# Optimization experiments

Measured on AMD Instinct MI355X. Metric: run time of the kernel, lower is better.

## Reference

```python
import jax, jax.numpy as jnp
import numpy as np

SQRT2 = np.float32(np.sqrt(2.0))


def _depthwise(x, h, axis):
    """Symmetric-pad depthwise 1D conv along `axis` (2=col/height, 3=row/width).
    Emulates dtcwt_slim ColFilter/RowFilter: prep_filt flips the taps, then
    F.conv2d cross-correlates with groups=C (same taps for every channel).
    x: (B,C,H,W), h: (L,) with L odd -> same-size output."""
    C = x.shape[1]
    L = h.shape[0]
    m = L // 2
    hf = jnp.flip(h)  # prep_filt stores h[::-1]
    if axis == 2:
        xp = jnp.pad(x, ((0, 0), (0, 0), (m, m), (0, 0)), mode='symmetric')
        ker = jnp.tile(hf[None, None, :, None], (C, 1, 1, 1))  # (C,1,L,1)
    else:
        xp = jnp.pad(x, ((0, 0), (0, 0), (0, 0), (m, m)), mode='symmetric')
        ker = jnp.tile(hf[None, None, None, :], (C, 1, 1, 1))  # (C,1,1,L)
    return jax.lax.conv_general_dilated(
        xp, ker, window_strides=(1, 1), padding='VALID',
        dimension_numbers=('NCHW', 'OIHW', 'NCHW'), feature_group_count=C)


def colfilter(x, h):
    return _depthwise(x, h, axis=2)


def rowfilter(x, h):
    return _depthwise(x, h, axis=3)


def c2q(w_r, w_i):
    """Complex pair of subbands -> real quad-interleaved image.
    w_r, w_i: (B,C,2,H,W) -> (B,C,2H,2W)."""
    w1r, w1i = w_r[:, :, 0], w_i[:, :, 0]
    w2r, w2i = w_r[:, :, 1], w_i[:, :, 1]
    x1 = w1r + w2r          # y[::2,  ::2]
    x2 = w1i + w2i          # y[::2, 1::2]
    x3 = w1i - w2i          # y[1::2, ::2]
    x4 = w2r - w1r          # y[1::2,1::2]
    B, C, H, W = x1.shape
    top = jnp.stack([x1, x2], axis=-1).reshape(B, C, H, 2 * W)
    bot = jnp.stack([x3, x4], axis=-1).reshape(B, C, H, 2 * W)
    y = jnp.stack([top, bot], axis=-2).reshape(B, C, 2 * H, 2 * W)
    return y / SQRT2


def setup_inputs() -> dict:
    key = jax.random.key(0)
    k1, k2, k3, k4, k5, k6 = jax.random.split(key, 6)
    B, C, H, W = 8, 64, 256, 256
    Yl = jax.random.normal(k1, (B, C, H, W), dtype=jnp.float32)
    Yhr = jax.random.normal(k2, (B, C, 6, H // 2, W // 2), dtype=jnp.float32)
    Yhi = jax.random.normal(k3, (B, C, 6, H // 2, W // 2), dtype=jnp.float32)
    # near_sym_b_bp synthesis filters (fixed, non-trainable buffers): 13/19/13 taps
    g0o = jax.random.normal(k4, (13,), dtype=jnp.float32) * 0.3
    g1o = jax.random.normal(k5, (19,), dtype=jnp.float32) * 0.3
    g2o = jax.random.normal(k6, (13,), dtype=jnp.float32) * 0.3
    return {"Yl": Yl, "Yhr": Yhr, "Yhi": Yhi, "g0o": g0o, "g1o": g1o, "g2o": g2o}


def reference(Yl, Yhr, Yhi, g0o, g1o, g2o):
    # orientation pairs: (15,165)->lh uses bands 0,5; (75,105)->hl bands 2,3;
    # (45,135 bandpass)->hh bands 1,4
    lh = c2q(Yhr[:, :, 0:6:5], Yhi[:, :, 0:6:5])
    hl = c2q(Yhr[:, :, 2:4:1], Yhi[:, :, 2:4:1])
    hh = c2q(Yhr[:, :, 1:5:3], Yhi[:, :, 1:5:3])
    y1 = colfilter(Yl, g0o) + colfilter(lh, g1o)
    y2 = colfilter(hl, g0o)
    y2bp = colfilter(hh, g2o)
    y = rowfilter(y1, g0o) + rowfilter(y2, g1o) + rowfilter(y2bp, g2o)
    return y
```

## Files before the change

### kernel.cpp

```cpp
#include <hip/hip_runtime.h>

#define TH 32
#define TW 64
#define PW 88

__device__ __forceinline__ int symidx(int t, int n) {
    t = (t < 0) ? (-1 - t) : t;
    return (t >= n) ? (2 * n - 1 - t) : t;
}

__device__ __forceinline__ void col13_yl(
    float (&acc)[TH], const float* __restrict__ ylp,
    const float (&taps)[13], int r0, int cc)
{
    #pragma unroll
    for (int pi = 0; pi < TH + 12; ++pi) {
        int rr = symidx(r0 - 6 + pi, 256);
        float v = ylp[rr * 256 + cc];
        #pragma unroll
        for (int j = 0; j < 13; ++j) {
            int ro = pi + j - 12;
            if (ro >= 0 && ro < TH) acc[ro] = fmaf(taps[j], v, acc[ro]);
        }
    }
}

__device__ __forceinline__ void col13_c2q(
    float (&acc)[TH], const float* __restrict__ yhr, const float* __restrict__ yhi,
    int bA, int bB, const float (&taps)[13], int r0, int cc)
{
    const int cp = cc & 1;
    const int j2 = cc >> 1;
    const float IS2 = 0.70710678118654752f;
    #pragma unroll
    for (int pi = 0; pi < TH + 12; ++pi) {
        int rr = symidx(r0 - 6 + pi, 256);
        int rp = rr & 1;
        int i2 = rr >> 1;
        const float* base = (((rp ^ cp) != 0) ? yhi : yhr) + (i2 * 128 + j2);
        float A  = base[bA * 16384];
        float Bv = base[bB * 16384];
        float vA = (rp & cp)       ? -A  : A;
        float vB = (rp & (cp ^ 1)) ? -Bv : Bv;
        float v = (vA + vB) * IS2;
        #pragma unroll
        for (int j = 0; j < 13; ++j) {
            int ro = pi + j - 12;
            if (ro >= 0 && ro < TH) acc[ro] = fmaf(taps[j], v, acc[ro]);
        }
    }
}

__device__ __forceinline__ void col19_c2q(
    float (&acc)[TH], const float* __restrict__ yhr, const float* __restrict__ yhi,
    const float (&taps)[19], int r0, int cc)
{
    const int bA = 0, bB = 5;
    const int cp = cc & 1;
    const int j2 = cc >> 1;
    const float IS2 = 0.70710678118654752f;
    #pragma unroll
    for (int pi = 0; pi < TH + 18; ++pi) {
        int rr = symidx(r0 - 9 + pi, 256);
        int rp = rr & 1;
        int i2 = rr >> 1;
        const float* base = (((rp ^ cp) != 0) ? yhi : yhr) + (i2 * 128 + j2);
        float A  = base[bA * 16384];
        float Bv = base[bB * 16384];
        float vA = (rp & cp)       ? -A  : A;
        float vB = (rp & (cp ^ 1)) ? -Bv : Bv;
        float v = (vA + vB) * IS2;
        #pragma unroll
        for (int j = 0; j < 19; ++j) {
            int ro = pi + j - 18;
            if (ro >= 0 && ro < TH) acc[ro] = fmaf(taps[j], v, acc[ro]);
        }
    }
}

extern "C" __global__ __launch_bounds__(512) void dtcwt_inv(
    const float* __restrict__ Yl, const float* __restrict__ Yhr,
    const float* __restrict__ Yhi,
    const float* __restrict__ g0, const float* __restrict__ g1,
    const float* __restrict__ g2, float* __restrict__ out)
{
    __shared__ __align__(16) float sT[4][TH][PW];

    const int tid = threadIdx.x;
    const int plane = blockIdx.z;
    const int r0 = blockIdx.y * TH;
    const int c0 = blockIdx.x * TW;

    const float* ylp = Yl  + (size_t)plane * 65536;
    const float* yhr = Yhr + (size_t)plane * 6 * 16384;
    const float* yhi = Yhi + (size_t)plane * 6 * 16384;

    float G0[13], G1[19], G2[13];
    #pragma unroll
    for (int j = 0; j < 13; ++j) G0[j] = g0[j];
    #pragma unroll
    for (int j = 0; j < 19; ++j) G1[j] = g1[j];
    #pragma unroll
    for (int j = 0; j < 13; ++j) G2[j] = g2[j];

    const int role = tid >> 7;
    const int lr   = tid & 127;

    float acc[TH];
    #pragma unroll
    for (int i = 0; i < TH; ++i) acc[i] = 0.0f;

    int ti = -1;
    if (role == 0) {
        if (lr < 76) {
            ti = lr + 6;
            int cc = symidx(c0 + ti - 12, 256);
            col13_yl(acc, ylp, G0, r0, cc);
        }
    } else if (role == 1) {
        if (lr < 76) {
            ti = lr + 6;
            int cc = symidx(c0 + ti - 12, 256);
            col19_c2q(acc, yhr, yhi, G1, r0, cc);
        }
    } else if (role == 2) {
        if (lr < 82) {
            ti = lr + 3;
            int cc = symidx(c0 + ti - 12, 256);
            col13_c2q(acc, yhr, yhi, 2, 3, G0, r0, cc);
        }
    } else {
        if (lr < 76) {
            ti = lr + 6;
            int cc = symidx(c0 + ti - 12, 256);
            col13_c2q(acc, yhr, yhi, 1, 4, G2, r0, cc);
        }
    }
    if (ti >= 0) {
        #pragma unroll
        for (int ro = 0; ro < TH; ++ro) sT[role][ro][ti] = acc[ro];
    }
    __syncthreads();

    const int cg = tid & 15;
    const int r  = tid >> 4;
    const int cb = 4 * cg;

    float w1[20];
    #pragma unroll
    for (int k = 0; k < 5; ++k) {
        float4 a = *(const float4*)&sT[0][r][cb + 4 + 4 * k];
        float4 b = *(const float4*)&sT[1][r][cb + 4 + 4 * k];
        w1[4*k+0] = a.x + b.x; w1[4*k+1] = a.y + b.y;
        w1[4*k+2] = a.z + b.z; w1[4*k+3] = a.w + b.w;
    }
    float w2[28];
    #pragma unroll
    for (int k = 0; k < 7; ++k) {
        float4 a = *(const float4*)&sT[2][r][cb + 4 * k];
        w2[4*k+0] = a.x; w2[4*k+1] = a.y; w2[4*k+2] = a.z; w2[4*k+3] = a.w;
    }
    float w3[20];
    #pragma unroll
    for (int k = 0; k < 5; ++k) {
        float4 a = *(const float4*)&sT[3][r][cb + 4 + 4 * k];
        w3[4*k+0] = a.x; w3[4*k+1] = a.y; w3[4*k+2] = a.z; w3[4*k+3] = a.w;
    }

    float4 res;
    float* rp = (float*)&res;
    #pragma unroll
    for (int q = 0; q < 4; ++q) {
        float s = 0.0f;
        #pragma unroll
        for (int j = 0; j < 13; ++j) s = fmaf(G0[j], w1[q + 14 - j], s);
        #pragma unroll
        for (int j = 0; j < 19; ++j) s = fmaf(G1[j], w2[q + 21 - j], s);
        #pragma unroll
        for (int j = 0; j < 13; ++j) s = fmaf(G2[j], w3[q + 14 - j], s);
        rp[q] = s;
    }
    *(float4*)&out[(size_t)plane * 65536 + (size_t)(r0 + r) * 256 + (c0 + cb)] = res;
}

extern "C" void kernel_launch(void* const* d_in, const int* in_sizes, int n_in,
                              void* d_out, int out_size, void* d_ws, size_t ws_size,
                              hipStream_t stream) {
    const float* Yl  = (const float*)d_in[0];
    const float* Yhr = (const float*)d_in[1];
    const float* Yhi = (const float*)d_in[2];
    const float* g0  = (const float*)d_in[3];
    const float* g1  = (const float*)d_in[4];
    const float* g2  = (const float*)d_in[5];
    float* out = (float*)d_out;

    dim3 grid(256 / TW, 256 / TH, 8 * 64);
    dim3 block(512, 1, 1);
    dtcwt_inv<<<grid, block, 0, stream>>>(Yl, Yhr, Yhi, g0, g1, g2, out);
}
```

Baseline: 351.2 us.

## Add interior-row fast path computing column pairs per thread with shared c2q loads

For row tiles away from the image border, each thread now computes two adjacent columns. For Yl it loads float2 pairs. For the c2q subbands it loads each of the four complex values once and reuses them for both row parities and both column parities, which removes the per-row symmetric indexing and repeated gathers. Filter taps are read directly from global memory instead of being copied into register arrays, which lowers register pressure but may add scalar loads. Border tiles keep the original path. Each active thread now holds two 32-element accumulator arrays, which raises register use, and only about 38 to 42 of the 64 threads in each of four waves do work.

```diff
diff --git a/kernel.cpp b/kernel.cpp
--- a/kernel.cpp
+++ b/kernel.cpp
@@ -3,6 +3,7 @@
 #define TH 32
 #define TW 64
 #define PW 88
+#define IS2 0.70710678118654752f
 
 __device__ __forceinline__ int symidx(int t, int n) {
     t = (t < 0) ? (-1 - t) : t;
@@ -11,7 +12,7 @@
 
 __device__ __forceinline__ void col13_yl(
     float (&acc)[TH], const float* __restrict__ ylp,
-    const float (&taps)[13], int r0, int cc)
+    const float* __restrict__ taps, int r0, int cc)
 {
     #pragma unroll
     for (int pi = 0; pi < TH + 12; ++pi) {
@@ -27,11 +28,10 @@
 
 __device__ __forceinline__ void col13_c2q(
     float (&acc)[TH], const float* __restrict__ yhr, const float* __restrict__ yhi,
-    int bA, int bB, const float (&taps)[13], int r0, int cc)
+    int bA, int bB, const float* __restrict__ taps, int r0, int cc)
 {
     const int cp = cc & 1;
     const int j2 = cc >> 1;
-    const float IS2 = 0.70710678118654752f;
     #pragma unroll
     for (int pi = 0; pi < TH + 12; ++pi) {
         int rr = symidx(r0 - 6 + pi, 256);
@@ -53,12 +53,11 @@
 
 __device__ __forceinline__ void col19_c2q(
     float (&acc)[TH], const float* __restrict__ yhr, const float* __restrict__ yhi,
-    const float (&taps)[19], int r0, int cc)
+    const float* __restrict__ taps, int r0, int cc)
 {
     const int bA = 0, bB = 5;
     const int cp = cc & 1;
     const int j2 = cc >> 1;
-    const float IS2 = 0.70710678118654752f;
     #pragma unroll
     for (int pi = 0; pi < TH + 18; ++pi) {
         int rr = symidx(r0 - 9 + pi, 256);
@@ -78,6 +77,62 @@
     }
 }
 
+template<int L, int NP, int EPI0>
+__device__ __forceinline__ void c2q_col_fast(
+    float (&accE)[TH], float (&accO)[TH],
+    const float* __restrict__ pRA, const float* __restrict__ pRB,
+    const float* __restrict__ pIA, const float* __restrict__ pIB,
+    int vof, const float* __restrict__ taps)
+{
+    #pragma unroll
+    for (int u = 0; u < NP; ++u) {
+        float Ar = pRA[vof + u * 128];
+        float Br = pRB[vof + u * 128];
+        float Ai = pIA[vof + u * 128];
+        float Bi = pIB[vof + u * 128];
+        float cee = (Ar + Br) * IS2;
+        float coe = (Ai + Bi) * IS2;
+        float ceo = (Ai - Bi) * IS2;
+        float coo = (Br - Ar) * IS2;
+        const int piE = EPI0 + 2 * u;
+        #pragma unroll
+        for (int j = 0; j < L; ++j) {
+            int ro = piE + j - (L - 1);
+            if (ro >= 0 && ro < TH) {
+                accE[ro] = fmaf(taps[j], cee, accE[ro]);
+                accO[ro] = fmaf(taps[j], coe, accO[ro]);
+            }
+        }
+        #pragma unroll
+        for (int j = 0; j < L; ++j) {
+            int ro = piE + 1 + j - (L - 1);
+            if (ro >= 0 && ro < TH) {
+                accE[ro] = fmaf(taps[j], ceo, accE[ro]);
+                accO[ro] = fmaf(taps[j], coo, accO[ro]);
+            }
+        }
+    }
+}
+
+__device__ __forceinline__ void yl_col_fast(
+    float (&accX)[TH], float (&accY)[TH],
+    const float* __restrict__ ylp, int rbase, int lo,
+    const float* __restrict__ taps)
+{
+    #pragma unroll
+    for (int pi = 0; pi < TH + 12; ++pi) {
+        float2 v = *(const float2*)&ylp[(rbase + pi) * 256 + lo];
+        #pragma unroll
+        for (int j = 0; j < 13; ++j) {
+            int ro = pi + j - 12;
+            if (ro >= 0 && ro < TH) {
+                accX[ro] = fmaf(taps[j], v.x, accX[ro]);
+                accY[ro] = fmaf(taps[j], v.y, accY[ro]);
+            }
+        }
+    }
+}
+
 extern "C" __global__ __launch_bounds__(512) void dtcwt_inv(
     const float* __restrict__ Yl, const float* __restrict__ Yhr,
     const float* __restrict__ Yhi,
@@ -95,50 +150,126 @@
     const float* yhr = Yhr + (size_t)plane * 6 * 16384;
     const float* yhi = Yhi + (size_t)plane * 6 * 16384;
 
-    float G0[13], G1[19], G2[13];
-    #pragma unroll
-    for (int j = 0; j < 13; ++j) G0[j] = g0[j];
-    #pragma unroll
-    for (int j = 0; j < 19; ++j) G1[j] = g1[j];
-    #pragma unroll
-    for (int j = 0; j < 13; ++j) G2[j] = g2[j];
-
-    const int role = tid >> 7;
-    const int lr   = tid & 127;
-
-    float acc[TH];
-    #pragma unroll
-    for (int i = 0; i < TH; ++i) acc[i] = 0.0f;
-
-    int ti = -1;
-    if (role == 0) {
-        if (lr < 76) {
-            ti = lr + 6;
-            int cc = symidx(c0 + ti - 12, 256);
-            col13_yl(acc, ylp, G0, r0, cc);
-        }
-    } else if (role == 1) {
-        if (lr < 76) {
-            ti = lr + 6;
-            int cc = symidx(c0 + ti - 12, 256);
-            col19_c2q(acc, yhr, yhi, G1, r0, cc);
-        }
-    } else if (role == 2) {
-        if (lr < 82) {
-            ti = lr + 3;
-            int cc = symidx(c0 + ti - 12, 256);
-            col13_c2q(acc, yhr, yhi, 2, 3, G0, r0, cc);
+    const bool rowInterior = (blockIdx.y >= 1) && (blockIdx.y <= 6);
+
+    if (rowInterior) {
+        const int w = tid >> 6;
+        const int p = tid & 63;
+        if (w == 0) {
+            if (p < 38) {
+                int e0 = c0 - 6 + 2 * p;
+                int s0 = symidx(e0, 256);
+                int s1 = symidx(e0 + 1, 256);
+                int lo = (s0 < s1) ? s0 : s1;
+                float accX[TH], accY[TH];
+                #pragma unroll
+                for (int i = 0; i < TH; ++i) { accX[i] = 0.f; accY[i] = 0.f; }
+                yl_col_fast(accX, accY, ylp, r0 - 6, lo, g0);
+                int ti0 = 6 + 2 * p;
+                int sw = (s0 == lo) ? 0 : 1;
+                #pragma unroll
+                for (int ro = 0; ro < TH; ++ro) {
+                    sT[0][ro][ti0 + sw]     = accX[ro];
+                    sT[0][ro][ti0 + 1 - sw] = accY[ro];
+                }
+            }
+        } else if (w == 1) {
+            if (p < 38) {
+                int e0 = c0 - 6 + 2 * p;
+                int s0 = symidx(e0, 256);
+                int j2 = s0 >> 1;
+                int q0 = s0 & 1;
+                float accE[TH], accO[TH];
+                #pragma unroll
+                for (int i = 0; i < TH; ++i) { accE[i] = 0.f; accO[i] = 0.f; }
+                int vof = ((r0 - 10) >> 1) * 128 + j2;
+                c2q_col_fast<19, 26, -1>(accE, accO,
+                    yhr + 0 * 16384, yhr + 5 * 16384,
+                    yhi + 0 * 16384, yhi + 5 * 16384, vof, g1);
+                int ti0 = 6 + 2 * p;
+                #pragma unroll
+                for (int ro = 0; ro < TH; ++ro) {
+                    sT[1][ro][ti0 + q0]     = accE[ro];
+                    sT[1][ro][ti0 + 1 - q0] = accO[ro];
+                }
+            }
+        } else if (w == 2) {
+            if (p < 42) {
+                int e0 = c0 - 10 + 2 * p;
+                int s0 = symidx(e0, 256);
+                int j2 = s0 >> 1;
+                int q0 = s0 & 1;
+                float accE[TH], accO[TH];
+                #pragma unroll
+                for (int i = 0; i < TH; ++i) { accE[i] = 0.f; accO[i] = 0.f; }
+                int vof = ((r0 - 6) >> 1) * 128 + j2;
+                c2q_col_fast<13, 22, 0>(accE, accO,
+                    yhr + 2 * 16384, yhr + 3 * 16384,
+                    yhi + 2 * 16384, yhi + 3 * 16384, vof, g0);
+                int ti0 = 2 + 2 * p;
+                #pragma unroll
+                for (int ro = 0; ro < TH; ++ro) {
+                    sT[2][ro][ti0 + q0]     = accE[ro];
+                    sT[2][ro][ti0 + 1 - q0] = accO[ro];
+                }
+            }
+        } else if (w == 3) {
+            if (p < 38) {
+                int e0 = c0 - 6 + 2 * p;
+                int s0 = symidx(e0, 256);
+                int j2 = s0 >> 1;
+                int q0 = s0 & 1;
+                float accE[TH], accO[TH];
+                #pragma unroll
+                for (int i = 0; i < TH; ++i) { accE[i] = 0.f; accO[i] = 0.f; }
+                int vof = ((r0 - 6) >> 1) * 128 + j2;
+                c2q_col_fast<13, 22, 0>(accE, accO,
+                    yhr + 1 * 16384, yhr + 4 * 16384,
+                    yhi + 1 * 16384, yhi + 4 * 16384, vof, g2);
+                int ti0 = 6 + 2 * p;
+                #pragma unroll
+                for (int ro = 0; ro < TH; ++ro) {
+                    sT[3][ro][ti0 + q0]     = accE[ro];
+                    sT[3][ro][ti0 + 1 - q0] = accO[ro];
+                }
+            }
         }
     } else {
-        if (lr < 76) {
-            ti = lr + 6;
-            int cc = symidx(c0 + ti - 12, 256);
-            col13_c2q(acc, yhr, yhi, 1, 4, G2, r0, cc);
-        }
-    }
-    if (ti >= 0) {
-        #pragma unroll
-        for (int ro = 0; ro < TH; ++ro) sT[role][ro][ti] = acc[ro];
+        const int role = tid >> 7;
+        const int lr   = tid & 127;
+        float acc[TH];
+        #pragma unroll
+        for (int i = 0; i < TH; ++i) acc[i] = 0.0f;
+        int ti = -1;
+        if (role == 0) {
+            if (lr < 76) {
+                ti = lr + 6;
+                int cc = symidx(c0 + ti - 12, 256);
+                col13_yl(acc, ylp, g0, r0, cc);
+            }
+        } else if (role == 1) {
+            if (lr < 76) {
+                ti = lr + 6;
+                int cc = symidx(c0 + ti - 12, 256);
+                col19_c2q(acc, yhr, yhi, g1, r0, cc);
+            }
+        } else if (role == 2) {
+            if (lr < 82) {
+                ti = lr + 3;
+                int cc = symidx(c0 + ti - 12, 256);
+                col13_c2q(acc, yhr, yhi, 2, 3, g0, r0, cc);
+            }
+        } else {
+            if (lr < 76) {
+                ti = lr + 6;
+                int cc = symidx(c0 + ti - 12, 256);
+                col13_c2q(acc, yhr, yhi, 1, 4, g2, r0, cc);
+            }
+        }
+        if (ti >= 0) {
+            #pragma unroll
+            for (int ro = 0; ro < TH; ++ro) sT[role][ro][ti] = acc[ro];
+        }
     }
     __syncthreads();
 
@@ -173,11 +304,11 @@
     for (int q = 0; q < 4; ++q) {
         float s = 0.0f;
         #pragma unroll
-        for (int j = 0; j < 13; ++j) s = fmaf(G0[j], w1[q + 14 - j], s);
-        #pragma unroll
-        for (int j = 0; j < 19; ++j) s = fmaf(G1[j], w2[q + 21 - j], s);
-        #pragma unroll
-        for (int j = 0; j < 13; ++j) s = fmaf(G2[j], w3[q + 14 - j], s);
+        for (int j = 0; j < 13; ++j) s = fmaf(g0[j], w1[q + 14 - j], s);
+        #pragma unroll
+        for (int j = 0; j < 19; ++j) s = fmaf(g1[j], w2[q + 21 - j], s);
+        #pragma unroll
+        for (int j = 0; j < 13; ++j) s = fmaf(g2[j], w3[q + 14 - j], s);
         rp[q] = s;
     }
     *(float4*)&out[(size_t)plane * 65536 + (size_t)(r0 + r) * 256 + (c0 + cb)] = res;
```

After: 440.4 us. 1.25x slower.

## Add interior-row fast path without symmetric index math for column filters

Applied to the files above, without the earlier changes.

Blocks whose row range is away from the image border (tile rows 1-6) now take a specialised column-filter path. It drops the per-row symmetric-index computation and the per-element yhr/yhi selects, and processes c2q rows in even/odd pairs with fixed pointers and a sign factor. Filter taps are read directly from global memory (uniform loads) instead of being cached in register arrays, which may lower register pressure. The cost is larger code and a second, divergent-by-block path that must stay consistent with the border path.

```diff
diff --git a/kernel.cpp b/kernel.cpp
--- a/kernel.cpp
+++ b/kernel.cpp
@@ -3,6 +3,7 @@
 #define TH 32
 #define TW 64
 #define PW 88
+#define IS2 0.70710678118654752f
 
 __device__ __forceinline__ int symidx(int t, int n) {
     t = (t < 0) ? (-1 - t) : t;
@@ -11,7 +12,7 @@
 
 __device__ __forceinline__ void col13_yl(
     float (&acc)[TH], const float* __restrict__ ylp,
-    const float (&taps)[13], int r0, int cc)
+    const float* __restrict__ taps, int r0, int cc)
 {
     #pragma unroll
     for (int pi = 0; pi < TH + 12; ++pi) {
@@ -27,11 +28,10 @@
 
 __device__ __forceinline__ void col13_c2q(
     float (&acc)[TH], const float* __restrict__ yhr, const float* __restrict__ yhi,
-    int bA, int bB, const float (&taps)[13], int r0, int cc)
+    int bA, int bB, const float* __restrict__ taps, int r0, int cc)
 {
     const int cp = cc & 1;
     const int j2 = cc >> 1;
-    const float IS2 = 0.70710678118654752f;
     #pragma unroll
     for (int pi = 0; pi < TH + 12; ++pi) {
         int rr = symidx(r0 - 6 + pi, 256);
@@ -53,12 +53,11 @@
 
 __device__ __forceinline__ void col19_c2q(
     float (&acc)[TH], const float* __restrict__ yhr, const float* __restrict__ yhi,
-    const float (&taps)[19], int r0, int cc)
+    const float* __restrict__ taps, int r0, int cc)
 {
     const int bA = 0, bB = 5;
     const int cp = cc & 1;
     const int j2 = cc >> 1;
-    const float IS2 = 0.70710678118654752f;
     #pragma unroll
     for (int pi = 0; pi < TH + 18; ++pi) {
         int rr = symidx(r0 - 9 + pi, 256);
@@ -78,6 +77,34 @@
     }
 }
 
+template<int L, int NP, int EPI0>
+__device__ __forceinline__ void c2q_col_fast1(
+    float (&acc)[TH],
+    const float* __restrict__ pEA, const float* __restrict__ pEB,
+    const float* __restrict__ pOA, const float* __restrict__ pOB,
+    int vof, float sgn, const float* __restrict__ taps)
+{
+    #pragma unroll
+    for (int u = 0; u < NP; ++u) {
+        float Ae = pEA[vof + u * 128];
+        float Be = pEB[vof + u * 128];
+        float Ao = pOA[vof + u * 128];
+        float Bo = pOB[vof + u * 128];
+        float ve = (Ae + Be) * IS2;
+        float vo = (Ao - Bo) * sgn;
+        #pragma unroll
+        for (int j = 0; j < L; ++j) {
+            int ro = EPI0 + 2 * u + j - (L - 1);
+            if (ro >= 0 && ro < TH) acc[ro] = fmaf(taps[j], ve, acc[ro]);
+        }
+        #pragma unroll
+        for (int j = 0; j < L; ++j) {
+            int ro = EPI0 + 2 * u + 1 + j - (L - 1);
+            if (ro >= 0 && ro < TH) acc[ro] = fmaf(taps[j], vo, acc[ro]);
+        }
+    }
+}
+
 extern "C" __global__ __launch_bounds__(512) void dtcwt_inv(
     const float* __restrict__ Yl, const float* __restrict__ Yhr,
     const float* __restrict__ Yhi,
@@ -95,13 +122,7 @@
     const float* yhr = Yhr + (size_t)plane * 6 * 16384;
     const float* yhi = Yhi + (size_t)plane * 6 * 16384;
 
-    float G0[13], G1[19], G2[13];
-    #pragma unroll
-    for (int j = 0; j < 13; ++j) G0[j] = g0[j];
-    #pragma unroll
-    for (int j = 0; j < 19; ++j) G1[j] = g1[j];
-    #pragma unroll
-    for (int j = 0; j < 13; ++j) G2[j] = g2[j];
+    const bool rowInterior = (blockIdx.y >= 1) && (blockIdx.y <= 6);
 
     const int role = tid >> 7;
     const int lr   = tid & 127;
@@ -109,31 +130,89 @@
     float acc[TH];
     #pragma unroll
     for (int i = 0; i < TH; ++i) acc[i] = 0.0f;
-
     int ti = -1;
-    if (role == 0) {
-        if (lr < 76) {
-            ti = lr + 6;
-            int cc = symidx(c0 + ti - 12, 256);
-            col13_yl(acc, ylp, G0, r0, cc);
-        }
-    } else if (role == 1) {
-        if (lr < 76) {
-            ti = lr + 6;
-            int cc = symidx(c0 + ti - 12, 256);
-            col19_c2q(acc, yhr, yhi, G1, r0, cc);
-        }
-    } else if (role == 2) {
-        if (lr < 82) {
-            ti = lr + 3;
-            int cc = symidx(c0 + ti - 12, 256);
-            col13_c2q(acc, yhr, yhi, 2, 3, G0, r0, cc);
+
+    if (rowInterior) {
+        if (role == 0) {
+            if (lr < 76) {
+                ti = lr + 6;
+                int cc = symidx(c0 + lr - 6, 256);
+                const float* p = ylp + (r0 - 6) * 256 + cc;
+                #pragma unroll
+                for (int pi = 0; pi < TH + 12; ++pi) {
+                    float v = p[pi * 256];
+                    #pragma unroll
+                    for (int j = 0; j < 13; ++j) {
+                        int ro = pi + j - 12;
+                        if (ro >= 0 && ro < TH) acc[ro] = fmaf(g0[j], v, acc[ro]);
+                    }
+                }
+            }
+        } else if (role == 1) {
+            if (lr < 76) {
+                ti = lr + 6;
+                int cc = symidx(c0 + lr - 6, 256);
+                int cp = cc & 1, j2 = cc >> 1;
+                const float* pE = cp ? yhi : yhr;
+                const float* pO = cp ? yhr : yhi;
+                float sgn = cp ? -IS2 : IS2;
+                int vof = ((r0 - 10) >> 1) * 128 + j2;
+                c2q_col_fast1<19, 26, -1>(acc,
+                    pE + 0 * 16384, pE + 5 * 16384,
+                    pO + 0 * 16384, pO + 5 * 16384, vof, sgn, g1);
+            }
+        } else if (role == 2) {
+            if (lr < 82) {
+                ti = lr + 3;
+                int cc = symidx(c0 + lr - 9, 256);
+                int cp = cc & 1, j2 = cc >> 1;
+                const float* pE = cp ? yhi : yhr;
+                const float* pO = cp ? yhr : yhi;
+                float sgn = cp ? -IS2 : IS2;
+                int vof = ((r0 - 6) >> 1) * 128 + j2;
+                c2q_col_fast1<13, 22, 0>(acc,
+                    pE + 2 * 16384, pE + 3 * 16384,
+                    pO + 2 * 16384, pO + 3 * 16384, vof, sgn, g0);
+            }
+        } else {
+            if (lr < 76) {
+                ti = lr + 6;
+                int cc = symidx(c0 + lr - 6, 256);
+                int cp = cc & 1, j2 = cc >> 1;
+                const float* pE = cp ? yhi : yhr;
+                const float* pO = cp ? yhr : yhi;
+                float sgn = cp ? -IS2 : IS2;
+                int vof = ((r0 - 6) >> 1) * 128 + j2;
+                c2q_col_fast1<13, 22, 0>(acc,
+                    pE + 1 * 16384, pE + 4 * 16384,
+                    pO + 1 * 16384, pO + 4 * 16384, vof, sgn, g2);
+            }
         }
     } else {
-        if (lr < 76) {
-            ti = lr + 6;
-            int cc = symidx(c0 + ti - 12, 256);
-            col13_c2q(acc, yhr, yhi, 1, 4, G2, r0, cc);
+        if (role == 0) {
+            if (lr < 76) {
+                ti = lr + 6;
+                int cc = symidx(c0 + ti - 12, 256);
+                col13_yl(acc, ylp, g0, r0, cc);
+            }
+        } else if (role == 1) {
+            if (lr < 76) {
+                ti = lr + 6;
+                int cc = symidx(c0 + ti - 12, 256);
+                col19_c2q(acc, yhr, yhi, g1, r0, cc);
+            }
+        } else if (role == 2) {
+            if (lr < 82) {
+                ti = lr + 3;
+                int cc = symidx(c0 + ti - 12, 256);
+                col13_c2q(acc, yhr, yhi, 2, 3, g0, r0, cc);
+            }
+        } else {
+            if (lr < 76) {
+                ti = lr + 6;
+                int cc = symidx(c0 + ti - 12, 256);
+                col13_c2q(acc, yhr, yhi, 1, 4, g2, r0, cc);
+            }
         }
     }
     if (ti >= 0) {
@@ -173,11 +252,11 @@
     for (int q = 0; q < 4; ++q) {
         float s = 0.0f;
         #pragma unroll
-        for (int j = 0; j < 13; ++j) s = fmaf(G0[j], w1[q + 14 - j], s);
-        #pragma unroll
-        for (int j = 0; j < 19; ++j) s = fmaf(G1[j], w2[q + 21 - j], s);
-        #pragma unroll
-        for (int j = 0; j < 13; ++j) s = fmaf(G2[j], w3[q + 14 - j], s);
+        for (int j = 0; j < 13; ++j) s = fmaf(g0[j], w1[q + 14 - j], s);
+        #pragma unroll
+        for (int j = 0; j < 19; ++j) s = fmaf(g1[j], w2[q + 21 - j], s);
+        #pragma unroll
+        for (int j = 0; j < 13; ++j) s = fmaf(g2[j], w3[q + 14 - j], s);
         rp[q] = s;
     }
     *(float4*)&out[(size_t)plane * 65536 + (size_t)(r0 + r) * 256 + (c0 + cb)] = res;
```

Result: slower. 417.2 us (+18.8%).

## Stage column inputs through LDS with prefetch overlap and all threads computing

Applied to the files above, without the earlier changes.

Replaces the per-role column filter, where only about 300 of 512 threads each ran a 32-row register accumulation, with a cooperative scheme. All threads load each input tile (Yl, then the three c2q band pairs) into a shared staging buffer. Every thread then computes 4 output rows for one column from LDS. The next band's global loads are issued before the current band's compute, so memory latency overlaps with the filtering. This costs extra LDS traffic and several more __syncthreads, and the filter taps are now read from global memory instead of being held in registers.

```diff
diff --git a/kernel.cpp b/kernel.cpp
--- a/kernel.cpp
+++ b/kernel.cpp
@@ -1,79 +1,110 @@
 #include <hip/hip_runtime.h>
 
-#define TH 32
-#define TW 64
 #define PW 88
+#define SP 84
+#define NCOL 82
+#define IS2 0.70710678118654752f
 
 __device__ __forceinline__ int symidx(int t, int n) {
     t = (t < 0) ? (-1 - t) : t;
     return (t >= n) ? (2 * n - 1 - t) : t;
 }
 
-__device__ __forceinline__ void col13_yl(
-    float (&acc)[TH], const float* __restrict__ ylp,
-    const float (&taps)[13], int r0, int cc)
-{
-    #pragma unroll
-    for (int pi = 0; pi < TH + 12; ++pi) {
-        int rr = symidx(r0 - 6 + pi, 256);
-        float v = ylp[rr * 256 + cc];
-        #pragma unroll
-        for (int j = 0; j < 13; ++j) {
-            int ro = pi + j - 12;
-            if (ro >= 0 && ro < TH) acc[ro] = fmaf(taps[j], v, acc[ro]);
-        }
-    }
-}
-
-__device__ __forceinline__ void col13_c2q(
-    float (&acc)[TH], const float* __restrict__ yhr, const float* __restrict__ yhi,
-    int bA, int bB, const float (&taps)[13], int r0, int cc)
-{
-    const int cp = cc & 1;
-    const int j2 = cc >> 1;
-    const float IS2 = 0.70710678118654752f;
-    #pragma unroll
-    for (int pi = 0; pi < TH + 12; ++pi) {
-        int rr = symidx(r0 - 6 + pi, 256);
-        int rp = rr & 1;
-        int i2 = rr >> 1;
-        const float* base = (((rp ^ cp) != 0) ? yhi : yhr) + (i2 * 128 + j2);
-        float A  = base[bA * 16384];
-        float Bv = base[bB * 16384];
-        float vA = (rp & cp)       ? -A  : A;
-        float vB = (rp & (cp ^ 1)) ? -Bv : Bv;
-        float v = (vA + vB) * IS2;
-        #pragma unroll
-        for (int j = 0; j < 13; ++j) {
-            int ro = pi + j - 12;
-            if (ro >= 0 && ro < TH) acc[ro] = fmaf(taps[j], v, acc[ro]);
-        }
-    }
-}
-
-__device__ __forceinline__ void col19_c2q(
-    float (&acc)[TH], const float* __restrict__ yhr, const float* __restrict__ yhi,
-    const float (&taps)[19], int r0, int cc)
-{
-    const int bA = 0, bB = 5;
-    const int cp = cc & 1;
-    const int j2 = cc >> 1;
-    const float IS2 = 0.70710678118654752f;
-    #pragma unroll
-    for (int pi = 0; pi < TH + 18; ++pi) {
-        int rr = symidx(r0 - 9 + pi, 256);
-        int rp = rr & 1;
-        int i2 = rr >> 1;
-        const float* base = (((rp ^ cp) != 0) ? yhi : yhr) + (i2 * 128 + j2);
-        float A  = base[bA * 16384];
-        float Bv = base[bB * 16384];
-        float vA = (rp & cp)       ? -A  : A;
-        float vB = (rp & (cp ^ 1)) ? -Bv : Bv;
-        float v = (vA + vB) * IS2;
-        #pragma unroll
-        for (int j = 0; j < 19; ++j) {
-            int ro = pi + j - 18;
-            if (ro >= 0 && ro < TH) acc[ro] = fmaf(taps[j], v, acc[ro]);
+__device__ __forceinline__ void issue_yl(float (&st)[9], const float* __restrict__ ylp,
+                                         int tid, int r0, int c0)
+{
+    #pragma unroll
+    for (int s = 0; s < 8; ++s) {
+        int idx = tid + s * 512;
+        if (idx < 44 * NCOL) {
+            int er = idx / NCOL;
+            int cj = idx - er * NCOL;
+            int rr = symidx(r0 - 6 + er, 256);
+            int cc = symidx(c0 + cj - 9, 256);
+            st[s] = ylp[rr * 256 + cc];
+        }
+    }
+}
+
+template<int NR, int RO, int NS>
+__device__ __forceinline__ void issue_c2q(float (&sA)[9], float (&sB)[9],
+    const float* __restrict__ yhr, const float* __restrict__ yhi,
+    int bA, int bB, int tid, int r0, int c0)
+{
+    #pragma unroll
+    for (int s = 0; s < NS; ++s) {
+        int idx = tid + s * 512;
+        if (idx < NR * NCOL) {
+            int er = idx / NCOL;
+            int cj = idx - er * NCOL;
+            int rr = symidx(r0 - RO + er, 256);
+            int cc = symidx(c0 + cj - 9, 256);
+            int rp = rr & 1, cp = cc & 1;
+            const float* base = (((rp ^ cp) != 0) ? yhi : yhr) + ((rr >> 1) * 128 + (cc >> 1));
+            sA[s] = base[bA * 16384];
+            sB[s] = base[bB * 16384];
+        }
+    }
+}
+
+__device__ __forceinline__ void write_yl(float* sIn, const float (&st)[9], int tid)
+{
+    #pragma unroll
+    for (int s = 0; s < 8; ++s) {
+        int idx = tid + s * 512;
+        if (idx < 44 * NCOL) {
+            int er = idx / NCOL;
+            int cj = idx - er * NCOL;
+            sIn[er * SP + cj] = st[s];
+        }
+    }
+}
+
+template<int NR, int RO, int NS>
+__device__ __forceinline__ void write_c2q(float* sIn, const float (&sA)[9], const float (&sB)[9],
+                                          int tid, int r0, int c0)
+{
+    #pragma unroll
+    for (int s = 0; s < NS; ++s) {
+        int idx = tid + s * 512;
+        if (idx < NR * NCOL) {
+            int er = idx / NCOL;
+            int cj = idx - er * NCOL;
+            int rp = symidx(r0 - RO + er, 256) & 1;
+            int cp = symidx(c0 + cj - 9, 256) & 1;
+            float A = sA[s], B = sB[s];
+            float vA = (rp & cp) ? -A : A;
+            float vB = (rp & (cp ^ 1)) ? -B : B;
+            sIn[er * SP + cj] = (vA + vB) * IS2;
+        }
+    }
+}
+
+template<int L>
+__device__ __forceinline__ void col_compute(float* sTk, const float* sIn,
+                                            const float* __restrict__ taps, int tid)
+{
+    #pragma unroll
+    for (int pass = 0; pass < 2; ++pass) {
+        int idx = tid + pass * 512;
+        if (idx < 8 * NCOL) {
+            int g  = idx / NCOL;
+            int cj = idx - g * NCOL;
+            int R  = 4 * g;
+            const float* q = sIn + R * SP + cj;
+            float a0 = 0.f, a1 = 0.f, a2 = 0.f, a3 = 0.f;
+            #pragma unroll
+            for (int t = 0; t < L + 3; ++t) {
+                float v = q[t * SP];
+                if (t < L)              a0 = fmaf(taps[L - 1 - t], v, a0);
+                if (t >= 1 && t < L+1)  a1 = fmaf(taps[L     - t], v, a1);
+                if (t >= 2 && t < L+2)  a2 = fmaf(taps[L + 1 - t], v, a2);
+                if (t >= 3)             a3 = fmaf(taps[L + 2 - t], v, a3);
+            }
+            sTk[(R + 0) * PW + cj + 3] = a0;
+            sTk[(R + 1) * PW + cj + 3] = a1;
+            sTk[(R + 2) * PW + cj + 3] = a2;
+            sTk[(R + 3) * PW + cj + 3] = a3;
         }
     }
 }
@@ -84,62 +115,43 @@
     const float* __restrict__ g0, const float* __restrict__ g1,
     const float* __restrict__ g2, float* __restrict__ out)
 {
-    __shared__ __align__(16) float sT[4][TH][PW];
+    __shared__ __align__(16) float sT[4][32][PW];
+    __shared__ __align__(16) float sIn[50 * SP];
 
     const int tid = threadIdx.x;
     const int plane = blockIdx.z;
-    const int r0 = blockIdx.y * TH;
-    const int c0 = blockIdx.x * TW;
+    const int r0 = blockIdx.y * 32;
+    const int c0 = blockIdx.x * 64;
 
     const float* ylp = Yl  + (size_t)plane * 65536;
     const float* yhr = Yhr + (size_t)plane * 6 * 16384;
     const float* yhi = Yhi + (size_t)plane * 6 * 16384;
 
-    float G0[13], G1[19], G2[13];
-    #pragma unroll
-    for (int j = 0; j < 13; ++j) G0[j] = g0[j];
-    #pragma unroll
-    for (int j = 0; j < 19; ++j) G1[j] = g1[j];
-    #pragma unroll
-    for (int j = 0; j < 13; ++j) G2[j] = g2[j];
-
-    const int role = tid >> 7;
-    const int lr   = tid & 127;
-
-    float acc[TH];
-    #pragma unroll
-    for (int i = 0; i < TH; ++i) acc[i] = 0.0f;
-
-    int ti = -1;
-    if (role == 0) {
-        if (lr < 76) {
-            ti = lr + 6;
-            int cc = symidx(c0 + ti - 12, 256);
-            col13_yl(acc, ylp, G0, r0, cc);
-        }
-    } else if (role == 1) {
-        if (lr < 76) {
-            ti = lr + 6;
-            int cc = symidx(c0 + ti - 12, 256);
-            col19_c2q(acc, yhr, yhi, G1, r0, cc);
-        }
-    } else if (role == 2) {
-        if (lr < 82) {
-            ti = lr + 3;
-            int cc = symidx(c0 + ti - 12, 256);
-            col13_c2q(acc, yhr, yhi, 2, 3, G0, r0, cc);
-        }
-    } else {
-        if (lr < 76) {
-            ti = lr + 6;
-            int cc = symidx(c0 + ti - 12, 256);
-            col13_c2q(acc, yhr, yhi, 1, 4, G2, r0, cc);
-        }
-    }
-    if (ti >= 0) {
-        #pragma unroll
-        for (int ro = 0; ro < TH; ++ro) sT[role][ro][ti] = acc[ro];
-    }
+    float stA[9], stB[9];
+
+    issue_yl(stA, ylp, tid, r0, c0);
+    write_yl(sIn, stA, tid);
+    __syncthreads();
+
+    issue_c2q<50, 9, 9>(stA, stB, yhr, yhi, 0, 5, tid, r0, c0);
+    col_compute<13>(&sT[0][0][0], sIn, g0, tid);
+    __syncthreads();
+    write_c2q<50, 9, 9>(sIn, stA, stB, tid, r0, c0);
+    __syncthreads();
+
+    issue_c2q<44, 6, 8>(stA, stB, yhr, yhi, 2, 3, tid, r0, c0);
+    col_compute<19>(&sT[1][0][0], sIn, g1, tid);
+    __syncthreads();
+    write_c2q<44, 6, 8>(sIn, stA, stB, tid, r0, c0);
+    __syncthreads();
+
+    issue_c2q<44, 6, 8>(stA, stB, yhr, yhi, 1, 4, tid, r0, c0);
+    col_compute<13>(&sT[2][0][0], sIn, g0, tid);
+    __syncthreads();
+    write_c2q<44, 6, 8>(sIn, stA, stB, tid, r0, c0);
+    __syncthreads();
+
+    col_compute<13>(&sT[3][0][0], sIn, g2, tid);
     __syncthreads();
 
     const int cg = tid & 15;
@@ -173,11 +185,11 @@
     for (int q = 0; q < 4; ++q) {
         float s = 0.0f;
         #pragma unroll
-        for (int j = 0; j < 13; ++j) s = fmaf(G0[j], w1[q + 14 - j], s);
+        for (int j = 0; j < 13; ++j) s = fmaf(g0[j], w1[q + 14 - j], s);
         #pragma unroll
-        for (int j = 0; j < 19; ++j) s = fmaf(G1[j], w2[q + 21 - j], s);
+        for (int j = 0; j < 19; ++j) s = fmaf(g1[j], w2[q + 21 - j], s);
         #pragma unroll
-        for (int j = 0; j < 13; ++j) s = fmaf(G2[j], w3[q + 14 - j], s);
+        for (int j = 0; j < 13; ++j) s = fmaf(g2[j], w3[q + 14 - j], s);
         rp[q] = s;
     }
     *(float4*)&out[(size_t)plane * 65536 + (size_t)(r0 + r) * 256 + (c0 + cb)] = res;
@@ -194,7 +206,7 @@
     const float* g2  = (const float*)d_in[5];
     float* out = (float*)d_out;
 
-    dim3 grid(256 / TW, 256 / TH, 8 * 64);
+    dim3 grid(256 / 64, 256 / 32, 8 * 64);
     dim3 block(512, 1, 1);
     dtcwt_inv<<<grid, block, 0, stream>>>(Yl, Yhr, Yhi, g0, g1, g2, out);
 }
```

After: 477.2 us. 1.36x slower.
